# Optimization experiments

Hardware: AMD Instinct MI355X
Metric: run time of the kernel (lower is better)

Reference implementation:

```python
import jax, jax.numpy as jnp
import numpy as np

NUM_GRAPHS = 64
N, E, H = 100000, 3200000, 64


def _glorot(k, shape):
    fan_in = shape[0]
    return jax.random.normal(k, shape, jnp.float32) * (1.0 / np.sqrt(fan_in))


def setup_inputs() -> dict:
    key = jax.random.key(0)
    ks = jax.random.split(key, 16)
    edge_index = jax.random.randint(ks[0], (2, E), 0, N)
    edge_weight = jax.random.uniform(ks[1], (E,), dtype=jnp.float32)
    batch = jnp.sort(jax.random.randint(ks[2], (N,), 0, NUM_GRAPHS))
    return {
        "edge_index": edge_index,
        "edge_weight": edge_weight,
        "batch": batch,
        "num_nodes": N,
        "W1": _glorot(ks[3], (1, H)), "b1": jnp.zeros((H,), jnp.float32),
        "W2": _glorot(ks[4], (H, H)), "b2": jnp.zeros((H,), jnp.float32),
        "W3": _glorot(ks[5], (H, H)), "b3": jnp.zeros((H,), jnp.float32),
        "W4": _glorot(ks[6], (H, H)), "b4": jnp.zeros((H,), jnp.float32),
        "W5": _glorot(ks[7], (H, H)), "b5": jnp.zeros((H,), jnp.float32),
        "lin_w": _glorot(ks[8], (H, 1)), "lin_b": jnp.zeros((1,), jnp.float32),
    }


def _gcn_layer(x, W, b, src, dst, w, n):
    # GCNConv(normalize=False): linear transform then weighted scatter-add over edges.
    h = x @ W                                  # [N, H]
    m = h[src] * w[:, None]                    # [E, H] messages
    return jax.ops.segment_sum(m, dst, num_segments=n) + b


def reference(edge_index, edge_weight, batch, num_nodes,
              W1, b1, W2, b2, W3, b3, W4, b4, W5, b5, lin_w, lin_b):
    src, dst = edge_index[0], edge_index[1]
    x = jnp.ones((num_nodes, 1), jnp.float32)
    for W, b in ((W1, b1), (W2, b2), (W3, b3), (W4, b4), (W5, b5)):
        x = jax.nn.relu(_gcn_layer(x, W, b, src, dst, edge_weight, num_nodes))
        # dropout p=0.1 is identity in eval mode
    # global mean pool per graph
    sums = jax.ops.segment_sum(x, batch, num_segments=NUM_GRAPHS)      # [G, H]
    counts = jax.ops.segment_sum(jnp.ones((num_nodes,), x.dtype), batch,
                                 num_segments=NUM_GRAPHS)
    pooled = sums / jnp.maximum(counts, 1.0)[:, None]
    return pooled @ lin_w + lin_b                                      # [G, 1]
```

## Files before the change

kernel.cpp:

```cpp
#include <hip/hip_runtime.h>

#define H 64
#define NUM_GRAPHS 64
#define BSHIFT 8
#define BSIZE 256
#define MAXNB 512
#define CHUNK 8192
#define BKT 9216
#define PADE 8
#define CSRB (BKT + BSIZE * PADE)
#define RPB 16

typedef unsigned int uint;
typedef unsigned short ushort;
typedef __attribute__((ext_vector_type(4))) float f32x4;
typedef __attribute__((ext_vector_type(8))) short short8;

__device__ __forceinline__ float bf2f(ushort u) {
    return __uint_as_float(((uint)u) << 16);
}
__device__ __forceinline__ ushort f2bf(float f) {
    uint b = __float_as_uint(f);
    b += 0x7FFFu + ((b >> 16) & 1u);
    return (ushort)(b >> 16);
}

__global__ void init_kernel(int* __restrict__ bucketCur, int NB) {
    int i = blockIdx.x * 256 + threadIdx.x;
    if (i < NB) bucketCur[i] = i * BKT;
}

__global__ __launch_bounds__(1024) void part_kernel(const int* __restrict__ src,
        const int* __restrict__ dst, const float* __restrict__ w,
        int* __restrict__ bucketCur, int2* __restrict__ bucketed, int E, int NB) {
    __shared__ int h[MAXNB];
    __shared__ int basev[MAXNB];
    __shared__ int lbase[MAXNB + 1];
    __shared__ int s[512];
    __shared__ int2 stage[CHUNK];
    int tid = threadIdx.x;
    for (int i = tid; i < NB; i += 1024) h[i] = 0;
    __syncthreads();
    int cbase = blockIdx.x * CHUNK;
    int cend = min(cbase + CHUNK, E);
    for (int e = cbase + tid; e < cend; e += 1024)
        atomicAdd(&h[dst[e] >> BSHIFT], 1);
    __syncthreads();
    for (int i = tid; i < NB; i += 1024) {
        int c = h[i];
        basev[i] = c ? atomicAdd(&bucketCur[i], c) : 0;
    }
    if (tid < 512) s[tid] = (tid < NB) ? h[tid] : 0;
    __syncthreads();
    for (int off = 1; off < 512; off <<= 1) {
        int t = (tid < 512 && tid >= off) ? s[tid - off] : 0;
        __syncthreads();
        if (tid < 512) s[tid] += t;
        __syncthreads();
    }
    if (tid < NB) lbase[tid + 1] = s[tid];
    if (tid == 0) lbase[0] = 0;
    __syncthreads();
    for (int i = tid; i < NB; i += 1024) h[i] = 0;
    __syncthreads();
    for (int e = cbase + tid; e < cend; e += 1024) {
        int d = dst[e];
        int b = d >> BSHIFT;
        int slot = atomicAdd(&h[b], 1);
        stage[lbase[b] + slot] =
            make_int2(((d & (BSIZE - 1)) << 17) | src[e], __float_as_int(w[e]));
    }
    __syncthreads();
    int lane = tid & 63, wv = tid >> 6;
    for (int b = wv; b < NB; b += 16) {
        int lb = lbase[b], cnt = lbase[b + 1] - lb, gb = basev[b];
        int lim = (b + 1) * BKT;
        for (int k = lane; k < cnt; k += 64)
            if (gb + k < lim) bucketed[gb + k] = stage[lb + k];
    }
}

__global__ __launch_bounds__(512) void bsort_kernel(const int* __restrict__ bucketCur,
        const int2* __restrict__ bucketed, uint* __restrict__ csr,
        int2* __restrict__ rowinfo, float* __restrict__ degw, int N) {
    __shared__ int cnt[BSIZE];
    __shared__ int pos[BSIZE];
    __shared__ int cur[BSIZE];
    __shared__ float wsum[BSIZE];
    int b = blockIdx.x;
    int tid = threadIdx.x;
    int nodeBase = b << BSHIFT;
    int nNodes = min(BSIZE, N - nodeBase);
    if (tid < BSIZE) { cnt[tid] = 0; wsum[tid] = 0.f; }
    __syncthreads();
    int ebeg = b * BKT;
    int eend = min(bucketCur[b], ebeg + BKT);
    for (int e = ebeg + tid; e < eend; e += 512)
        atomicAdd(&cnt[bucketed[e].x >> 17], 1);
    __syncthreads();
    int pc = 0;
    if (tid < BSIZE) { pc = (cnt[tid] + PADE - 1) & ~(PADE - 1); pos[tid] = pc; }
    __syncthreads();
    for (int off = 1; off < BSIZE; off <<= 1) {
        int t = (tid < BSIZE && tid >= off) ? pos[tid - off] : 0;
        __syncthreads();
        if (tid < BSIZE) pos[tid] += t;
        __syncthreads();
    }
    int csrBase = b * CSRB;
    if (tid < BSIZE) {
        int excl = pos[tid] - pc;
        cur[tid] = excl;
        if (tid < nNodes) rowinfo[nodeBase + tid] = make_int2(csrBase + excl, pc);
    }
    __syncthreads();
    for (int e = ebeg + tid; e < eend; e += 512) {
        int2 v = bucketed[e];
        int dl = v.x >> 17;
        int slot = atomicAdd(&cur[dl], 1);
        uint wb = (uint)v.y;
        wb += 0x7FFFu + ((wb >> 16) & 1u);
        uint w15 = (wb >> 16) & 0x7FFFu;
        csr[csrBase + slot] = (((uint)(v.x & 0x1FFFF)) << 15) | w15;
        atomicAdd(&wsum[dl], __uint_as_float(w15 << 16));
    }
    __syncthreads();
    if (tid < nNodes) {
        degw[nodeBase + tid] = wsum[tid];
        int e0 = cur[tid];
        int e1 = pos[tid];
        for (int k = e0; k < e1; ++k) csr[csrBase + k] = 0u;
    }
}

__global__ void layer1_kernel(const float* __restrict__ degw, const float* __restrict__ W1,
                              const float* __restrict__ b1, ushort* __restrict__ out, int N) {
    int gid = blockIdx.x * 256 + threadIdx.x;
    if (gid >= N * 16) return;
    int i = gid >> 4, c4 = (gid & 15) * 4;
    float d = degw[i];
    uint lo = (uint)f2bf(fmaxf(d * W1[c4 + 0] + b1[c4 + 0], 0.f))
            | ((uint)f2bf(fmaxf(d * W1[c4 + 1] + b1[c4 + 1], 0.f)) << 16);
    uint hi = (uint)f2bf(fmaxf(d * W1[c4 + 2] + b1[c4 + 2], 0.f))
            | ((uint)f2bf(fmaxf(d * W1[c4 + 3] + b1[c4 + 3], 0.f)) << 16);
    *reinterpret_cast<uint2*>(out + ((size_t)i << 6) + c4) = make_uint2(lo, hi);
}

__global__ void count_kernel(const int* __restrict__ batch, float* __restrict__ gcnt, int N) {
    __shared__ int bins[NUM_GRAPHS];
    int tid = threadIdx.x;
    if (tid < NUM_GRAPHS) bins[tid] = 0;
    __syncthreads();
    int node = blockIdx.x * 256 + tid;
    if (node < N) atomicAdd(&bins[batch[node]], 1);
    __syncthreads();
    if (tid < NUM_GRAPHS && bins[tid])
        unsafeAtomicAdd(&gcnt[tid], (float)bins[tid]);
}

template<bool LAST>
__global__ __launch_bounds__(256) void layer_kernel(const int2* __restrict__ rowinfo,
        const uint* __restrict__ csr, const ushort* __restrict__ x,
        const float* __restrict__ W, const float* __restrict__ bvec,
        ushort* __restrict__ out, const int* __restrict__ batch,
        const float* __restrict__ linw, float* __restrict__ gsum, int N) {
    __shared__ alignas(16) ushort Wt[64][72];
    __shared__ alignas(16) ushort AG[RPB][72];
    __shared__ float gbins[NUM_GRAPHS];
    int tid = threadIdx.x;
    for (int i = tid; i < 64 * 64; i += 256) {
        int k = i >> 6, c = i & 63;
        Wt[c][k] = f2bf(W[i]);
    }
    if (LAST && tid < NUM_GRAPHS) gbins[tid] = 0.f;
    __syncthreads();
    int lane = tid & 63, wid = tid >> 6;
    int half4 = (lane >> 5) << 2;
    const char* xb = (const char*)x + (size_t)((lane & 31) << 2);
    int rowbase = blockIdx.x * RPB;
#pragma unroll 1
    for (int p = 0; p < 4; ++p) {
        int trow = wid * 4 + p;
        int row = rowbase + trow;
        float a0 = 0.f, a1 = 0.f;
        if (row < N) {
            int2 ri = rowinfo[row];
            int beg = ri.x, lenp = ri.y;
            uint pv = (lane < lenp) ? __builtin_nontemporal_load(csr + beg + lane) : 0u;
#pragma unroll 1
            for (int ck = 0; ck < lenp; ck += 64) {
                uint pvn = 0u;
                int nidx = ck + 64 + lane;
                if (nidx < lenp)
                    pvn = __builtin_nontemporal_load(csr + beg + nidx);
                int ng = min(64, lenp - ck) >> 1;
#pragma unroll 1
                for (int g = 0; g < ng; g += 4) {
                    uint p0 = (uint)__builtin_amdgcn_ds_bpermute(8 * g + half4, (int)pv);
                    uint p1 = (uint)__builtin_amdgcn_ds_bpermute(8 * g + 8 + half4, (int)pv);
                    uint p2 = (uint)__builtin_amdgcn_ds_bpermute(8 * g + 16 + half4, (int)pv);
                    uint p3 = (uint)__builtin_amdgcn_ds_bpermute(8 * g + 24 + half4, (int)pv);
                    uint u0 = *reinterpret_cast<const uint*>(xb + ((size_t)(p0 >> 15) << 7));
                    uint u1 = *reinterpret_cast<const uint*>(xb + ((size_t)(p1 >> 15) << 7));
                    uint u2 = *reinterpret_cast<const uint*>(xb + ((size_t)(p2 >> 15) << 7));
                    uint u3 = *reinterpret_cast<const uint*>(xb + ((size_t)(p3 >> 15) << 7));
                    float w0 = __uint_as_float((p0 & 0x7FFFu) << 16);
                    float w1 = __uint_as_float((p1 & 0x7FFFu) << 16);
                    float w2 = __uint_as_float((p2 & 0x7FFFu) << 16);
                    float w3 = __uint_as_float((p3 & 0x7FFFu) << 16);
                    a0 = fmaf(w0, __uint_as_float(u0 << 16), a0);
                    a1 = fmaf(w0, __uint_as_float(u0 & 0xFFFF0000u), a1);
                    a0 = fmaf(w1, __uint_as_float(u1 << 16), a0);
                    a1 = fmaf(w1, __uint_as_float(u1 & 0xFFFF0000u), a1);
                    a0 = fmaf(w2, __uint_as_float(u2 << 16), a0);
                    a1 = fmaf(w2, __uint_as_float(u2 & 0xFFFF0000u), a1);
                    a0 = fmaf(w3, __uint_as_float(u3 << 16), a0);
                    a1 = fmaf(w3, __uint_as_float(u3 & 0xFFFF0000u), a1);
                }
                pv = pvn;
            }
        }
        a0 += __shfl_xor(a0, 32);
        a1 += __shfl_xor(a1, 32);
        if (lane < 32) {
            uint pk = (uint)f2bf(a0) | ((uint)f2bf(a1) << 16);
            *reinterpret_cast<uint*>(&AG[trow][lane << 1]) = pk;
        }
    }
    __syncthreads();
    int cl = lane & 15, kg = lane >> 4;
    int c0 = wid * 16;
    short8 a0v = *reinterpret_cast<const short8*>(&AG[cl][kg * 8]);
    short8 a1v = *reinterpret_cast<const short8*>(&AG[cl][32 + kg * 8]);
    short8 bb0 = *reinterpret_cast<const short8*>(&Wt[c0 + cl][kg * 8]);
    short8 bb1 = *reinterpret_cast<const short8*>(&Wt[c0 + cl][32 + kg * 8]);
    f32x4 acc = {0.f, 0.f, 0.f, 0.f};
    acc = __builtin_amdgcn_mfma_f32_16x16x32_bf16(a0v, bb0, acc, 0, 0, 0);
    acc = __builtin_amdgcn_mfma_f32_16x16x32_bf16(a1v, bb1, acc, 0, 0, 0);
    float bias = bvec[c0 + cl];
    float lw = LAST ? linw[c0 + cl] : 0.f;
#pragma unroll
    for (int j = 0; j < 4; ++j) {
        int r = rowbase + kg * 4 + j;
        if (r < N) {
            float v = fmaxf(acc[j] + bias, 0.f);
            if (!LAST)
                __builtin_nontemporal_store(f2bf(v), out + ((size_t)r << 6) + c0 + cl);
            else
                atomicAdd(&gbins[batch[r]], v * lw);
        }
    }
    if (LAST) {
        __syncthreads();
        if (tid < NUM_GRAPHS) unsafeAtomicAdd(&gsum[tid], gbins[tid]);
    }
}

__global__ void final_kernel(const float* __restrict__ gsum, const float* __restrict__ gcnt,
                             const float* __restrict__ lin_b, float* __restrict__ out) {
    int g = threadIdx.x;
    if (g < NUM_GRAPHS) out[g] = gsum[g] / fmaxf(gcnt[g], 1.f) + lin_b[0];
}

extern "C" void kernel_launch(void* const* d_in, const int* in_sizes, int n_in,
                              void* d_out, int out_size, void* d_ws, size_t ws_size,
                              hipStream_t stream) {
    const int*   edge_index = (const int*)d_in[0];
    const float* ew    = (const float*)d_in[1];
    const int*   batch = (const int*)d_in[2];
    const float* W1    = (const float*)d_in[4];
    const float* b1    = (const float*)d_in[5];
    const float* Wl[4] = {(const float*)d_in[6], (const float*)d_in[8],
                          (const float*)d_in[10], (const float*)d_in[12]};
    const float* bl[4] = {(const float*)d_in[7], (const float*)d_in[9],
                          (const float*)d_in[11], (const float*)d_in[13]};
    const float* linw  = (const float*)d_in[14];
    const float* linb  = (const float*)d_in[15];

    const int E = in_sizes[1];
    const int N = in_sizes[2];
    const int* src = edge_index;
    const int* dst = edge_index + E;
    const int NB = (N + BSIZE - 1) >> BSHIFT;

    char* base = (char*)d_ws;
    size_t featPad = (((size_t)(N + 16) * H * 2) + 255) & ~(size_t)255;
    size_t bktBytes = (((size_t)NB * BKT * 8) + 255) & ~(size_t)255;
    size_t span = 2 * featPad > bktBytes ? 2 * featPad : bktBytes;
    ushort* bufA = (ushort*)base;
    ushort* bufB = (ushort*)(base + featPad);
    int2* bucketed = (int2*)base;
    uint* csr = (uint*)(base + span);
    size_t csrBytes = (((size_t)NB * CSRB * 4) + 255) & ~(size_t)255;
    char* tail = base + span + csrBytes;
    int2* rowinfo   = (int2*)tail;
    int* bucketCur  = (int*)(rowinfo + N);
    float* gsum     = (float*)(bucketCur + MAXNB);
    float* gcnt     = gsum + NUM_GRAPHS;
    float* degw     = gcnt + NUM_GRAPHS;

    const int chunks = (E + CHUNK - 1) / CHUNK;

    init_kernel<<<(NB + 255) / 256, 256, 0, stream>>>(bucketCur, NB);
    hipMemsetAsync(gsum, 0, 2 * NUM_GRAPHS * sizeof(float), stream);
    part_kernel<<<chunks, 1024, 0, stream>>>(src, dst, ew, bucketCur, bucketed, E, NB);
    bsort_kernel<<<NB, 512, 0, stream>>>(bucketCur, bucketed, csr, rowinfo, degw, N);

    layer1_kernel<<<(N * 16 + 255) / 256, 256, 0, stream>>>(degw, W1, b1, bufA, N);
    count_kernel<<<(N + 255) / 256, 256, 0, stream>>>(batch, gcnt, N);

    const int gridL = (N + RPB - 1) / RPB;
    ushort* xin = bufA;
    ushort* xout = bufB;
    for (int l = 0; l < 3; ++l) {
        layer_kernel<false><<<gridL, 256, 0, stream>>>(rowinfo, csr, xin, Wl[l], bl[l],
                xout, batch, linw, gsum, N);
        ushort* t = xin; xin = xout; xout = t;
    }
    layer_kernel<true><<<gridL, 256, 0, stream>>>(rowinfo, csr, xin, Wl[3], bl[3],
            xout, batch, linw, gsum, N);

    final_kernel<<<1, 64, 0, stream>>>(gsum, gcnt, linb, (float*)d_out);
}
```

Measured before the change: 454.4 us.

## Stage CSR entries in LDS, drop padding zero-fill, unroll gather with dual accumulators

The CSR build no longer zero-fills padded slots and stores the true row length instead of the padded one. The layer kernel loads each 64-entry chunk of packed edges into shared memory and reads them back as broadcasts, replacing ds_bpermute. The gather loop is fully unrolled over 8 groups, guarded by a group count, with two accumulator pairs to shorten FMA dependency chains. This removes the padding-write pass and the wasted gathers on padded zeros. In exchange it drops the prefetch of the next chunk and relies on same-wave LDS write/read ordering without an explicit barrier. Tail entries past len are loaded as zero, which points at row 0 with zero weight, so results stay correct.

```diff
diff --git a/kernel.cpp b/kernel.cpp
--- a/kernel.cpp
+++ b/kernel.cpp
@@ -111,7 +111,7 @@
     if (tid < BSIZE) {
         int excl = pos[tid] - pc;
         cur[tid] = excl;
-        if (tid < nNodes) rowinfo[nodeBase + tid] = make_int2(csrBase + excl, pc);
+        if (tid < nNodes) rowinfo[nodeBase + tid] = make_int2(csrBase + excl, cnt[tid]);
     }
     __syncthreads();
     for (int e = ebeg + tid; e < eend; e += 512) {
@@ -125,12 +125,7 @@
         atomicAdd(&wsum[dl], __uint_as_float(w15 << 16));
     }
     __syncthreads();
-    if (tid < nNodes) {
-        degw[nodeBase + tid] = wsum[tid];
-        int e0 = cur[tid];
-        int e1 = pos[tid];
-        for (int k = e0; k < e1; ++k) csr[csrBase + k] = 0u;
-    }
+    if (tid < nNodes) degw[nodeBase + tid] = wsum[tid];
 }
 
 __global__ void layer1_kernel(const float* __restrict__ degw, const float* __restrict__ W1,
@@ -166,6 +161,7 @@
         const float* __restrict__ linw, float* __restrict__ gsum, int N) {
     __shared__ alignas(16) ushort Wt[64][72];
     __shared__ alignas(16) ushort AG[RPB][72];
+    __shared__ uint pc[4][64];
     __shared__ float gbins[NUM_GRAPHS];
     int tid = threadIdx.x;
     for (int i = tid; i < 64 * 64; i += 256) {
@@ -175,51 +171,45 @@
     if (LAST && tid < NUM_GRAPHS) gbins[tid] = 0.f;
     __syncthreads();
     int lane = tid & 63, wid = tid >> 6;
-    int half4 = (lane >> 5) << 2;
+    int hi = lane >> 5;
     const char* xb = (const char*)x + (size_t)((lane & 31) << 2);
     int rowbase = blockIdx.x * RPB;
 #pragma unroll 1
     for (int p = 0; p < 4; ++p) {
         int trow = wid * 4 + p;
         int row = rowbase + trow;
-        float a0 = 0.f, a1 = 0.f;
+        float a0 = 0.f, a1 = 0.f, b0 = 0.f, b1 = 0.f;
         if (row < N) {
             int2 ri = rowinfo[row];
-            int beg = ri.x, lenp = ri.y;
-            uint pv = (lane < lenp) ? __builtin_nontemporal_load(csr + beg + lane) : 0u;
+            int beg = ri.x, len = ri.y;
 #pragma unroll 1
-            for (int ck = 0; ck < lenp; ck += 64) {
-                uint pvn = 0u;
-                int nidx = ck + 64 + lane;
-                if (nidx < lenp)
-                    pvn = __builtin_nontemporal_load(csr + beg + nidx);
-                int ng = min(64, lenp - ck) >> 1;
-#pragma unroll 1
-                for (int g = 0; g < ng; g += 4) {
-                    uint p0 = (uint)__builtin_amdgcn_ds_bpermute(8 * g + half4, (int)pv);
-                    uint p1 = (uint)__builtin_amdgcn_ds_bpermute(8 * g + 8 + half4, (int)pv);
-                    uint p2 = (uint)__builtin_amdgcn_ds_bpermute(8 * g + 16 + half4, (int)pv);
-                    uint p3 = (uint)__builtin_amdgcn_ds_bpermute(8 * g + 24 + half4, (int)pv);
-                    uint u0 = *reinterpret_cast<const uint*>(xb + ((size_t)(p0 >> 15) << 7));
-                    uint u1 = *reinterpret_cast<const uint*>(xb + ((size_t)(p1 >> 15) << 7));
-                    uint u2 = *reinterpret_cast<const uint*>(xb + ((size_t)(p2 >> 15) << 7));
-                    uint u3 = *reinterpret_cast<const uint*>(xb + ((size_t)(p3 >> 15) << 7));
-                    float w0 = __uint_as_float((p0 & 0x7FFFu) << 16);
-                    float w1 = __uint_as_float((p1 & 0x7FFFu) << 16);
-                    float w2 = __uint_as_float((p2 & 0x7FFFu) << 16);
-                    float w3 = __uint_as_float((p3 & 0x7FFFu) << 16);
-                    a0 = fmaf(w0, __uint_as_float(u0 << 16), a0);
-                    a1 = fmaf(w0, __uint_as_float(u0 & 0xFFFF0000u), a1);
-                    a0 = fmaf(w1, __uint_as_float(u1 << 16), a0);
-                    a1 = fmaf(w1, __uint_as_float(u1 & 0xFFFF0000u), a1);
-                    a0 = fmaf(w2, __uint_as_float(u2 << 16), a0);
-                    a1 = fmaf(w2, __uint_as_float(u2 & 0xFFFF0000u), a1);
-                    a0 = fmaf(w3, __uint_as_float(u3 << 16), a0);
-                    a1 = fmaf(w3, __uint_as_float(u3 & 0xFFFF0000u), a1);
+            for (int ck = 0; ck < len; ck += 64) {
+                int idx = ck + lane;
+                uint pv = (idx < len) ? __builtin_nontemporal_load(csr + beg + idx) : 0u;
+                pc[wid][lane] = pv;
+                int grps = (min(64, len - ck) + 7) >> 3;
+#pragma unroll
+                for (int g = 0; g < 8; ++g) {
+                    if (g < grps) {
+#pragma unroll
+                        for (int jp = 0; jp < 4; ++jp) {
+                            uint pp = pc[wid][g * 8 + jp * 2 + hi];
+                            uint u = *reinterpret_cast<const uint*>(
+                                         xb + ((size_t)(pp >> 15) << 7));
+                            float wf = __uint_as_float((pp & 0x7FFFu) << 16);
+                            if (g & 1) {
+                                b0 = fmaf(wf, __uint_as_float(u << 16), b0);
+                                b1 = fmaf(wf, __uint_as_float(u & 0xFFFF0000u), b1);
+                            } else {
+                                a0 = fmaf(wf, __uint_as_float(u << 16), a0);
+                                a1 = fmaf(wf, __uint_as_float(u & 0xFFFF0000u), a1);
+                            }
+                        }
+                    }
                 }
-                pv = pvn;
             }
         }
+        a0 += b0; a1 += b1;
         a0 += __shfl_xor(a0, 32);
         a1 += __shfl_xor(a1, 32);
         if (lane < 32) {
```

Result: slower. 470.0 us (+3.4%).
